# Kernel tuning notes

Measured on AMD Instinct MI355X. Metric: run time of the kernel, lower is better.

Reference implementation:

```python
import jax, jax.numpy as jnp
import numpy as np

N_NODES = 100000
N_EDGES = 1600000
D_IN = 128
D_OUT = 128


def setup_inputs() -> dict:
    key = jax.random.key(0)
    k_x, k_e, k_wl, k_bl, k_wr = jax.random.split(key, 5)
    x = jax.random.normal(k_x, (N_NODES, D_IN), dtype=jnp.float32)
    edge_index = jax.random.randint(k_e, (2, N_EDGES), 0, N_NODES, dtype=jnp.int64)
    s = 1.0 / np.sqrt(D_IN)
    W_l = jax.random.uniform(k_wl, (D_OUT, D_IN), minval=-s, maxval=s, dtype=jnp.float32)
    b_l = jax.random.uniform(k_bl, (D_OUT,), minval=-s, maxval=s, dtype=jnp.float32)
    W_r = jax.random.uniform(k_wr, (D_OUT, D_IN), minval=-s, maxval=s, dtype=jnp.float32)
    return {"x": x, "edge_index": edge_index, "W_l": W_l, "b_l": b_l, "W_r": W_r}


def reference(x, edge_index, W_l, b_l, W_r):
    # PyG SAGEConv with mean aggregation:
    #   out = lin_l(mean_{j in N(i)} x_j) + lin_r(x_i), followed by ReLU.
    src, dst = edge_index[0], edge_index[1]
    # gather source features [E, D_IN] and mean-aggregate at destinations
    msg_sum = jax.ops.segment_sum(x[src], dst, num_segments=N_NODES)  # [N, D_IN]
    deg = jax.ops.segment_sum(jnp.ones((edge_index.shape[1],), dtype=x.dtype), dst,
                              num_segments=N_NODES)  # [N]
    agg = msg_sum / jnp.maximum(deg, 1.0)[:, None]  # isolated nodes -> 0
    out = agg @ W_l.T + b_l + x @ W_r.T
    return jax.nn.relu(out)
```

## Files before the change

### kernel.cpp

```cpp
#include <hip/hip_runtime.h>
#include <hip/hip_bf16.h>
#include <cstddef>
#include <cstdint>

#define D 128
#define BCHUNK 4096
#define SLOTS 64
#define QTILE 64
#define LROW 68
#define GRAN 512
#define SBCAP 9728
#define NGMAX 256

typedef __bf16 bf16x8 __attribute__((ext_vector_type(8)));
typedef float  f32x4  __attribute__((ext_vector_type(4)));
typedef float  f32x2  __attribute__((ext_vector_type(2)));

__device__ __forceinline__ unsigned int f2bf(float f) {
    unsigned int u = __float_as_uint(f);
    return (u + 0x7FFFu + ((u >> 16) & 1u)) >> 16;
}

__global__ __launch_bounds__(256) void bucketx2_kernel(
    const int* __restrict__ ei, int E, int* __restrict__ subCnt,
    unsigned int* __restrict__ sub, int NG, int nbE, int nbX,
    const float4* __restrict__ x4, uint2* __restrict__ xb2,
    unsigned int* __restrict__ xg, int nq,
    const float* __restrict__ Wl, const float* __restrict__ Wr,
    const float* __restrict__ bl, unsigned short* __restrict__ bfrag,
    float* __restrict__ biasbuf)
{
    const int bid = blockIdx.x;
    if (bid >= nbE) {
        const int xi = bid - nbE;
        if (xi < nbX) {
            const int base = xi * 1024 + threadIdx.x;
            #pragma unroll
            for (int k = 0; k < 4; k++) {
                int i = base + k * 256;
                if (i < nq) {
                    float4 v = x4[i];
                    uint2 r;
                    r.x = f2bf(v.x) | (f2bf(v.y) << 16);
                    r.y = f2bf(v.z) | (f2bf(v.w) << 16);
                    xb2[i] = r;
                    int g = 0;
                    g = __builtin_amdgcn_cvt_pk_fp8_f32(v.x, v.y, g, false);
                    g = __builtin_amdgcn_cvt_pk_fp8_f32(v.z, v.w, g, true);
                    xg[(size_t)((i >> 5) + 1) * 32 + (i & 31)] = (unsigned int)g;
                }
            }
        } else {
            int f = (xi - nbX) * 256 + threadIdx.x;
            if (f < 4096) {
                int ct   = f >> 9;
                int q    = (f >> 6) & 7;
                int lane = f & 63;
                int o  = 16 * ct + (lane & 15);
                int kb = 32 * q + (lane >> 4) * 8;
                const float* s = (kb < 128) ? (Wl + (size_t)o * 128 + kb)
                                            : (Wr + (size_t)o * 128 + (kb - 128));
                uint4 u;
                u.x = f2bf(s[0]) | (f2bf(s[1]) << 16);
                u.y = f2bf(s[2]) | (f2bf(s[3]) << 16);
                u.z = f2bf(s[4]) | (f2bf(s[5]) << 16);
                u.w = f2bf(s[6]) | (f2bf(s[7]) << 16);
                reinterpret_cast<uint4*>(bfrag)[f] = u;
                if (f < 128) biasbuf[f] = bl[f];
                if (f < 32)  xg[f] = 0u;
            }
        }
        return;
    }
    __shared__ int cnt[NGMAX];
    __shared__ int basem[NGMAX];
    __shared__ int wsum[4];
    __shared__ unsigned int ebuf[BCHUNK];
    __shared__ unsigned int gpb[BCHUNK];

    for (int i = threadIdx.x; i < NG; i += 256) cnt[i] = 0;
    __syncthreads();
    const int cb = bid * BCHUNK;
    int srcs[16], gs[16], d9s[16];
    #pragma unroll
    for (int k = 0; k < 16; k++) {
        int e = cb + threadIdx.x + k * 256;
        bool v = e < E;
        srcs[k] = v ? ei[e] : 0;
        int dst = v ? ei[E + e] : 0;
        gs[k]  = v ? (dst >> 9) : -1;
        d9s[k] = dst & 511;
        if (v) atomicAdd(&cnt[gs[k]], 1);
    }
    __syncthreads();
    const int tid = threadIdx.x;
    int c = (tid < NG) ? cnt[tid] : 0;
    int gbase = (tid < NG && c > 0) ? atomicAdd(&subCnt[tid], c) : 0;
    int xsc = c;
    #pragma unroll
    for (int dd = 1; dd < 64; dd <<= 1) {
        int y = __shfl_up(xsc, dd);
        if ((tid & 63) >= dd) xsc += y;
    }
    if ((tid & 63) == 63) wsum[tid >> 6] = xsc;
    __syncthreads();
    int woff = 0;
    #pragma unroll
    for (int ww = 0; ww < 4; ww++)
        if (ww < (tid >> 6)) woff += wsum[ww];
    int pref = xsc - c + woff;
    __syncthreads();
    if (tid < NG) { cnt[tid] = pref; basem[tid] = gbase - pref; }
    __syncthreads();
    #pragma unroll
    for (int k = 0; k < 16; k++) {
        if (gs[k] >= 0) {
            int g  = gs[k];
            int lp = atomicAdd(&cnt[g], 1);
            int bp = basem[g] + lp;
            ebuf[lp] = (unsigned int)(srcs[k] + 1) | ((unsigned int)d9s[k] << 20);
            gpb[lp]  = (bp < SBCAP) ? (unsigned int)g * SBCAP + bp : 0xFFFFFFFFu;
        }
    }
    __syncthreads();
    const int nE = min(E - cb, BCHUNK);
    for (int i = tid; i < nE; i += 256) {
        unsigned int p = gpb[i];
        if (p != 0xFFFFFFFFu) sub[p] = ebuf[i];
    }
}

__global__ __launch_bounds__(512) void gathformer_kernel(
    const unsigned int* __restrict__ sub, const int* __restrict__ subCnt,
    const unsigned int* __restrict__ xg, const unsigned int* __restrict__ xb,
    const unsigned short* __restrict__ bfrag, const float* __restrict__ biasbuf,
    float* __restrict__ out, int N)
{
    __shared__ unsigned int lds[QTILE * LROW];
    __shared__ int lcsr[QTILE * SLOTS];
    __shared__ int lcnt[QTILE];

    const int g     = blockIdx.x >> 3;
    const int h     = blockIdx.x & 7;
    const int node0 = g * GRAN + (h << 6);

    const int w    = threadIdx.x >> 6;
    const int lane = threadIdx.x & 63;
    const int sb   = lane & 31;
    const int half = lane >> 5;

    if (threadIdx.x < QTILE) lcnt[threadIdx.x] = 0;
    __syncthreads();
    const int n = min(subCnt[g], SBCAP);
    const unsigned int* S = sub + (size_t)g * SBCAP;
    for (int bi = (int)threadIdx.x * 4; bi < n; bi += 2048) {
        uint4 e4 = *reinterpret_cast<const uint4*>(S + bi);
        #pragma unroll
        for (int j = 0; j < 4; j++) {
            unsigned int en = (&e4.x)[j];
            if (bi + j < n) {
                int d9 = (en >> 20) & 511;
                if ((d9 >> 6) == h) {
                    int ln  = d9 & 63;
                    int pos = atomicAdd(&lcnt[ln], 1);
                    if (pos < SLOTS) lcsr[ln * SLOTS + pos] = (int)(en & 0xFFFFFu);
                }
            }
        }
    }
    __syncthreads();

    const int imax = min(8, N - node0 - w * 8);
    #pragma unroll 2
    for (int i = 0; i < imax; i++) {
        int ln  = w * 8 + i;
        int deg = lcnt[ln];
        int dl  = min(deg, SLOTS);
        int nbatch = (dl + 15) >> 4;
        const int* nb = lcsr + ln * SLOTS;
        f32x2 a01 = {0.f, 0.f};
        f32x2 a23 = {0.f, 0.f};
        for (int b = 0; b < nbatch; b++) {
            const int j = b * 16;
            unsigned int v[8];
            #pragma unroll
            for (int u = 0; u < 8; u++) {
                int slot = j + 2 * u + half;
                int raw  = nb[slot];
                int s    = (slot < dl) ? raw : 0;
                v[u] = xg[(size_t)s * 32 + sb];
            }
            #pragma unroll
            for (int u = 0; u < 8; u++) {
                a01 += __builtin_amdgcn_cvt_pk_f32_fp8(v[u], false);
                a23 += __builtin_amdgcn_cvt_pk_f32_fp8(v[u], true);
            }
        }
        a01.x += __shfl_xor(a01.x, 32);
        a01.y += __shfl_xor(a01.y, 32);
        a23.x += __shfl_xor(a23.x, 32);
        a23.y += __shfl_xor(a23.y, 32);
        if (half == 0) {
            float inv = 1.0f / fmaxf((float)deg, 1.0f);
            int b = ln * LROW + sb * 2;
            lds[b]     = f2bf(a01.x * inv) | (f2bf(a01.y * inv) << 16);
            lds[b + 1] = f2bf(a23.x * inv) | (f2bf(a23.y * inv) << 16);
        }
    }
    __syncthreads();

    const int quad = lane >> 4;
    const int r15  = lane & 15;
    bf16x8 bw[8];
    #pragma unroll
    for (int q = 0; q < 8; q++)
        bw[q] = reinterpret_cast<const bf16x8*>(bfrag)[(w * 8 + q) * 64 + lane];
    const float bias = biasbuf[16 * w + r15];
    const int col = 16 * w + r15;

    #pragma unroll 1
    for (int mt = 0; mt < 4; mt++) {
        int rowbase = node0 + mt * 16;
        if (rowbase >= N) break;
        int rc = min(rowbase + r15, N - 1);
        f32x4 acc = {0.f, 0.f, 0.f, 0.f};
        const int lbase = (mt * 16 + r15) * LROW + quad * 4;
        #pragma unroll
        for (int q = 0; q < 4; q++) {
            bf16x8 a = *reinterpret_cast<const bf16x8*>(&lds[lbase + q * 16]);
            acc = __builtin_amdgcn_mfma_f32_16x16x32_bf16(a, bw[q], acc, 0, 0, 0);
        }
        const unsigned short* xrow =
            (const unsigned short*)xb + (size_t)rc * 128 + quad * 8;
        #pragma unroll
        for (int q = 4; q < 8; q++) {
            bf16x8 a = *reinterpret_cast<const bf16x8*>(xrow + (q - 4) * 32);
            acc = __builtin_amdgcn_mfma_f32_16x16x32_bf16(a, bw[q], acc, 0, 0, 0);
        }
        #pragma unroll
        for (int r = 0; r < 4; r++) {
            int orow = rowbase + quad * 4 + r;
            if (orow < N)
                out[(size_t)orow * D + col] = fmaxf(acc[r] + bias, 0.0f);
        }
    }
}

extern "C" void kernel_launch(void* const* d_in, const int* in_sizes, int n_in,
                              void* d_out, int out_size, void* d_ws, size_t ws_size,
                              hipStream_t stream)
{
    const float* x  = (const float*)d_in[0];
    const int*   ei = (const int*)d_in[1];
    const float* Wl = (const float*)d_in[2];
    const float* bl = (const float*)d_in[3];
    const float* Wr = (const float*)d_in[4];
    float* out = (float*)d_out;

    const int nodes = in_sizes[0] / D;
    const int E     = in_sizes[1] / 2;
    const int NG    = (nodes + GRAN - 1) / GRAN;

    unsigned int* xg = (unsigned int*)d_ws;
    unsigned int* xb = xg + (size_t)(nodes + 1) * 32;
    unsigned short* bfrag = (unsigned short*)(xb + (size_t)nodes * 64);
    float* biasbuf   = (float*)(bfrag + 4096 * 8);
    int* subCnt      = (int*)(biasbuf + 128);
    unsigned int* sub = (unsigned int*)(subCnt + 512);

    hipMemsetAsync(subCnt, 0, (size_t)NG * sizeof(int), stream);

    const int nbE = (E + BCHUNK - 1) / BCHUNK;
    const int nq  = nodes * 32;
    const int nbX = (nq + 1023) / 1024;
    bucketx2_kernel<<<nbE + nbX + 16, 256, 0, stream>>>(
        ei, E, subCnt, sub, NG, nbE, nbX,
        (const float4*)x, (uint2*)xb, xg, nq, Wl, Wr, bl, bfrag, biasbuf);

    gathformer_kernel<<<NG * 8, 512, 0, stream>>>(
        sub, subCnt, xg, xb, bfrag, biasbuf, out, nodes);
}
```

Before: 185.1 us.

## Replace atomic scatter bucketing with chunk-local sort plus deterministic regroup kernel

```diff
diff --git a/kernel.cpp b/kernel.cpp
--- a/kernel.cpp
+++ b/kernel.cpp
@@ -11,6 +11,8 @@
 #define GRAN 512
 #define SBCAP 9728
 #define NGMAX 256
+#define PSTRIDE 200
+#define NBEMAX 416
 
 typedef __bf16 bf16x8 __attribute__((ext_vector_type(8)));
 typedef float  f32x4  __attribute__((ext_vector_type(4)));
@@ -21,9 +23,9 @@
     return (u + 0x7FFFu + ((u >> 16) & 1u)) >> 16;
 }
 
-__global__ __launch_bounds__(256) void bucketx2_kernel(
-    const int* __restrict__ ei, int E, int* __restrict__ subCnt,
-    unsigned int* __restrict__ sub, int NG, int nbE, int nbX,
+__global__ __launch_bounds__(256) void prep_kernel(
+    const int* __restrict__ ei, int E, unsigned int* __restrict__ chunks,
+    unsigned short* __restrict__ pref, int NG, int nbE, int nbX,
     const float4* __restrict__ x4, uint2* __restrict__ xb2,
     unsigned int* __restrict__ xg, int nq,
     const float* __restrict__ Wl, const float* __restrict__ Wr,
@@ -73,14 +75,13 @@
         return;
     }
     __shared__ int cnt[NGMAX];
-    __shared__ int basem[NGMAX];
     __shared__ int wsum[4];
     __shared__ unsigned int ebuf[BCHUNK];
-    __shared__ unsigned int gpb[BCHUNK];
 
     for (int i = threadIdx.x; i < NG; i += 256) cnt[i] = 0;
     __syncthreads();
     const int cb = bid * BCHUNK;
+    const int nE = min(E - cb, BCHUNK);
     int srcs[16], gs[16], d9s[16];
     #pragma unroll
     for (int k = 0; k < 16; k++) {
@@ -95,7 +96,6 @@
     __syncthreads();
     const int tid = threadIdx.x;
     int c = (tid < NG) ? cnt[tid] : 0;
-    int gbase = (tid < NG && c > 0) ? atomicAdd(&subCnt[tid], c) : 0;
     int xsc = c;
     #pragma unroll
     for (int dd = 1; dd < 64; dd <<= 1) {
@@ -108,25 +108,67 @@
     #pragma unroll
     for (int ww = 0; ww < 4; ww++)
         if (ww < (tid >> 6)) woff += wsum[ww];
-    int pref = xsc - c + woff;
-    __syncthreads();
-    if (tid < NG) { cnt[tid] = pref; basem[tid] = gbase - pref; }
+    int pfx = xsc - c + woff;
+    if (tid < NG)  pref[(size_t)bid * PSTRIDE + tid] = (unsigned short)pfx;
+    if (tid == NG) pref[(size_t)bid * PSTRIDE + NG] = (unsigned short)nE;
+    __syncthreads();
+    if (tid < NG) cnt[tid] = pfx;
     __syncthreads();
     #pragma unroll
     for (int k = 0; k < 16; k++) {
         if (gs[k] >= 0) {
-            int g  = gs[k];
-            int lp = atomicAdd(&cnt[g], 1);
-            int bp = basem[g] + lp;
+            int lp = atomicAdd(&cnt[gs[k]], 1);
             ebuf[lp] = (unsigned int)(srcs[k] + 1) | ((unsigned int)d9s[k] << 20);
-            gpb[lp]  = (bp < SBCAP) ? (unsigned int)g * SBCAP + bp : 0xFFFFFFFFu;
-        }
-    }
-    __syncthreads();
-    const int nE = min(E - cb, BCHUNK);
-    for (int i = tid; i < nE; i += 256) {
-        unsigned int p = gpb[i];
-        if (p != 0xFFFFFFFFu) sub[p] = ebuf[i];
+        }
+    }
+    __syncthreads();
+    unsigned int* dst = chunks + (size_t)bid * BCHUNK;
+    #pragma unroll
+    for (int p = 0; p < 4; p++) {
+        int idx = p * 1024 + tid * 4;
+        uint4 v = *reinterpret_cast<const uint4*>(&ebuf[idx]);
+        *reinterpret_cast<uint4*>(&dst[idx]) = v;
+    }
+}
+
+__global__ __launch_bounds__(512) void regroup_kernel(
+    const unsigned int* __restrict__ chunks, const unsigned short* __restrict__ pref,
+    int nbE, unsigned int* __restrict__ sub, int* __restrict__ subCnt, int NG)
+{
+    __shared__ int s_start[NBEMAX], s_off[NBEMAX], s_len[NBEMAX];
+    __shared__ int wsumS[8];
+    const int g    = blockIdx.x;
+    const int tid  = threadIdx.x;
+    const int w    = tid >> 6;
+    const int lane = tid & 63;
+
+    int st = 0, len = 0;
+    if (tid < nbE) {
+        st  = pref[(size_t)tid * PSTRIDE + g];
+        len = pref[(size_t)tid * PSTRIDE + g + 1] - st;
+    }
+    int xsc = len;
+    #pragma unroll
+    for (int dd = 1; dd < 64; dd <<= 1) {
+        int y = __shfl_up(xsc, dd);
+        if (lane >= dd) xsc += y;
+    }
+    if (lane == 63) wsumS[w] = xsc;
+    __syncthreads();
+    int woff = 0;
+    #pragma unroll
+    for (int ww = 0; ww < 8; ww++)
+        if (ww < w) woff += wsumS[ww];
+    int off = xsc - len + woff;
+    if (tid < nbE) { s_start[tid] = st; s_off[tid] = off; s_len[tid] = len; }
+    if (tid == 511) subCnt[g] = off;
+    __syncthreads();
+
+    for (int b = w; b < nbE; b += 8) {
+        int bst = s_start[b], boff = s_off[b], bln = s_len[b];
+        const unsigned int* src = chunks + (size_t)b * BCHUNK + bst;
+        for (int o = lane; o < bln; o += 64)
+            if (boff + o < SBCAP) sub[(size_t)g * SBCAP + boff + o] = src[o];
     }
 }
 
@@ -260,22 +302,24 @@
     const int nodes = in_sizes[0] / D;
     const int E     = in_sizes[1] / 2;
     const int NG    = (nodes + GRAN - 1) / GRAN;
+    const int nbE   = (E + BCHUNK - 1) / BCHUNK;
 
     unsigned int* xg = (unsigned int*)d_ws;
     unsigned int* xb = xg + (size_t)(nodes + 1) * 32;
     unsigned short* bfrag = (unsigned short*)(xb + (size_t)nodes * 64);
     float* biasbuf   = (float*)(bfrag + 4096 * 8);
     int* subCnt      = (int*)(biasbuf + 128);
-    unsigned int* sub = (unsigned int*)(subCnt + 512);
-
-    hipMemsetAsync(subCnt, 0, (size_t)NG * sizeof(int), stream);
-
-    const int nbE = (E + BCHUNK - 1) / BCHUNK;
+    unsigned short* pref = (unsigned short*)(subCnt + 512);
+    unsigned int* chunks = (unsigned int*)(pref + (size_t)nbE * PSTRIDE);
+    unsigned int* sub    = chunks + (size_t)nbE * BCHUNK;
+
     const int nq  = nodes * 32;
     const int nbX = (nq + 1023) / 1024;
-    bucketx2_kernel<<<nbE + nbX + 16, 256, 0, stream>>>(
-        ei, E, subCnt, sub, NG, nbE, nbX,
+    prep_kernel<<<nbE + nbX + 16, 256, 0, stream>>>(
+        ei, E, chunks, pref, NG, nbE, nbX,
         (const float4*)x, (uint2*)xb, xg, nq, Wl, Wr, bl, bfrag, biasbuf);
+
+    regroup_kernel<<<NG, 512, 0, stream>>>(chunks, pref, nbE, sub, subCnt, NG);
 
     gathformer_kernel<<<NG * 8, 512, 0, stream>>>(
         sub, subCnt, xg, xb, bfrag, biasbuf, out, nodes);
```

New measurement: 206.8 us. 1.12x slower.

## Split fused bucket/cast kernel and make gather-transform kernel persistent

Applied to the files above, without the earlier changes.

```diff
diff --git a/kernel.cpp b/kernel.cpp
--- a/kernel.cpp
+++ b/kernel.cpp
@@ -11,6 +11,7 @@
 #define GRAN 512
 #define SBCAP 9728
 #define NGMAX 256
+#define GFGRID 1024
 
 typedef __bf16 bf16x8 __attribute__((ext_vector_type(8)));
 typedef float  f32x4  __attribute__((ext_vector_type(4)));
@@ -21,63 +22,64 @@
     return (u + 0x7FFFu + ((u >> 16) & 1u)) >> 16;
 }
 
-__global__ __launch_bounds__(256) void bucketx2_kernel(
-    const int* __restrict__ ei, int E, int* __restrict__ subCnt,
-    unsigned int* __restrict__ sub, int NG, int nbE, int nbX,
+__global__ __launch_bounds__(256) void xcast_kernel(
     const float4* __restrict__ x4, uint2* __restrict__ xb2,
-    unsigned int* __restrict__ xg, int nq,
+    unsigned int* __restrict__ xg, int nq, int nbX,
     const float* __restrict__ Wl, const float* __restrict__ Wr,
     const float* __restrict__ bl, unsigned short* __restrict__ bfrag,
     float* __restrict__ biasbuf)
 {
-    const int bid = blockIdx.x;
-    if (bid >= nbE) {
-        const int xi = bid - nbE;
-        if (xi < nbX) {
-            const int base = xi * 1024 + threadIdx.x;
-            #pragma unroll
-            for (int k = 0; k < 4; k++) {
-                int i = base + k * 256;
-                if (i < nq) {
-                    float4 v = x4[i];
-                    uint2 r;
-                    r.x = f2bf(v.x) | (f2bf(v.y) << 16);
-                    r.y = f2bf(v.z) | (f2bf(v.w) << 16);
-                    xb2[i] = r;
-                    int g = 0;
-                    g = __builtin_amdgcn_cvt_pk_fp8_f32(v.x, v.y, g, false);
-                    g = __builtin_amdgcn_cvt_pk_fp8_f32(v.z, v.w, g, true);
-                    xg[(size_t)((i >> 5) + 1) * 32 + (i & 31)] = (unsigned int)g;
-                }
-            }
-        } else {
-            int f = (xi - nbX) * 256 + threadIdx.x;
-            if (f < 4096) {
-                int ct   = f >> 9;
-                int q    = (f >> 6) & 7;
-                int lane = f & 63;
-                int o  = 16 * ct + (lane & 15);
-                int kb = 32 * q + (lane >> 4) * 8;
-                const float* s = (kb < 128) ? (Wl + (size_t)o * 128 + kb)
-                                            : (Wr + (size_t)o * 128 + (kb - 128));
-                uint4 u;
-                u.x = f2bf(s[0]) | (f2bf(s[1]) << 16);
-                u.y = f2bf(s[2]) | (f2bf(s[3]) << 16);
-                u.z = f2bf(s[4]) | (f2bf(s[5]) << 16);
-                u.w = f2bf(s[6]) | (f2bf(s[7]) << 16);
-                reinterpret_cast<uint4*>(bfrag)[f] = u;
-                if (f < 128) biasbuf[f] = bl[f];
-                if (f < 32)  xg[f] = 0u;
-            }
-        }
-        return;
-    }
+    const int xi = blockIdx.x;
+    if (xi < nbX) {
+        const int base = xi * 1024 + threadIdx.x;
+        #pragma unroll
+        for (int k = 0; k < 4; k++) {
+            int i = base + k * 256;
+            if (i < nq) {
+                float4 v = x4[i];
+                uint2 r;
+                r.x = f2bf(v.x) | (f2bf(v.y) << 16);
+                r.y = f2bf(v.z) | (f2bf(v.w) << 16);
+                xb2[i] = r;
+                int g = 0;
+                g = __builtin_amdgcn_cvt_pk_fp8_f32(v.x, v.y, g, false);
+                g = __builtin_amdgcn_cvt_pk_fp8_f32(v.z, v.w, g, true);
+                xg[(size_t)((i >> 5) + 1) * 32 + (i & 31)] = (unsigned int)g;
+            }
+        }
+    } else {
+        int f = (xi - nbX) * 256 + threadIdx.x;
+        if (f < 4096) {
+            int ct   = f >> 9;
+            int q    = (f >> 6) & 7;
+            int lane = f & 63;
+            int o  = 16 * ct + (lane & 15);
+            int kb = 32 * q + (lane >> 4) * 8;
+            const float* s = (kb < 128) ? (Wl + (size_t)o * 128 + kb)
+                                        : (Wr + (size_t)o * 128 + (kb - 128));
+            uint4 u;
+            u.x = f2bf(s[0]) | (f2bf(s[1]) << 16);
+            u.y = f2bf(s[2]) | (f2bf(s[3]) << 16);
+            u.z = f2bf(s[4]) | (f2bf(s[5]) << 16);
+            u.w = f2bf(s[6]) | (f2bf(s[7]) << 16);
+            reinterpret_cast<uint4*>(bfrag)[f] = u;
+            if (f < 128) biasbuf[f] = bl[f];
+            if (f < 32)  xg[f] = 0u;
+        }
+    }
+}
+
+__global__ __launch_bounds__(256) void edges_kernel(
+    const int* __restrict__ ei, int E, int* __restrict__ subCnt,
+    unsigned int* __restrict__ sub, int NG)
+{
     __shared__ int cnt[NGMAX];
     __shared__ int basem[NGMAX];
     __shared__ int wsum[4];
     __shared__ unsigned int ebuf[BCHUNK];
     __shared__ unsigned int gpb[BCHUNK];
 
+    const int bid = blockIdx.x;
     for (int i = threadIdx.x; i < NG; i += 256) cnt[i] = 0;
     __syncthreads();
     const int cb = bid * BCHUNK;
@@ -134,115 +136,119 @@
     const unsigned int* __restrict__ sub, const int* __restrict__ subCnt,
     const unsigned int* __restrict__ xg, const unsigned int* __restrict__ xb,
     const unsigned short* __restrict__ bfrag, const float* __restrict__ biasbuf,
-    float* __restrict__ out, int N)
+    float* __restrict__ out, int N, int ntiles)
 {
     __shared__ unsigned int lds[QTILE * LROW];
     __shared__ int lcsr[QTILE * SLOTS];
     __shared__ int lcnt[QTILE];
 
-    const int g     = blockIdx.x >> 3;
-    const int h     = blockIdx.x & 7;
-    const int node0 = g * GRAN + (h << 6);
-
-    const int w    = threadIdx.x >> 6;
-    const int lane = threadIdx.x & 63;
+    const int tid  = threadIdx.x;
+    const int w    = tid >> 6;
+    const int lane = tid & 63;
     const int sb   = lane & 31;
     const int half = lane >> 5;
-
-    if (threadIdx.x < QTILE) lcnt[threadIdx.x] = 0;
-    __syncthreads();
-    const int n = min(subCnt[g], SBCAP);
-    const unsigned int* S = sub + (size_t)g * SBCAP;
-    for (int bi = (int)threadIdx.x * 4; bi < n; bi += 2048) {
-        uint4 e4 = *reinterpret_cast<const uint4*>(S + bi);
-        #pragma unroll
-        for (int j = 0; j < 4; j++) {
-            unsigned int en = (&e4.x)[j];
-            if (bi + j < n) {
-                int d9 = (en >> 20) & 511;
-                if ((d9 >> 6) == h) {
-                    int ln  = d9 & 63;
-                    int pos = atomicAdd(&lcnt[ln], 1);
-                    if (pos < SLOTS) lcsr[ln * SLOTS + pos] = (int)(en & 0xFFFFFu);
-                }
-            }
-        }
-    }
-    __syncthreads();
-
-    const int imax = min(8, N - node0 - w * 8);
-    #pragma unroll 2
-    for (int i = 0; i < imax; i++) {
-        int ln  = w * 8 + i;
-        int deg = lcnt[ln];
-        int dl  = min(deg, SLOTS);
-        int nbatch = (dl + 15) >> 4;
-        const int* nb = lcsr + ln * SLOTS;
-        f32x2 a01 = {0.f, 0.f};
-        f32x2 a23 = {0.f, 0.f};
-        for (int b = 0; b < nbatch; b++) {
-            const int j = b * 16;
-            unsigned int v[8];
-            #pragma unroll
-            for (int u = 0; u < 8; u++) {
-                int slot = j + 2 * u + half;
-                int raw  = nb[slot];
-                int s    = (slot < dl) ? raw : 0;
-                v[u] = xg[(size_t)s * 32 + sb];
-            }
-            #pragma unroll
-            for (int u = 0; u < 8; u++) {
-                a01 += __builtin_amdgcn_cvt_pk_f32_fp8(v[u], false);
-                a23 += __builtin_amdgcn_cvt_pk_f32_fp8(v[u], true);
-            }
-        }
-        a01.x += __shfl_xor(a01.x, 32);
-        a01.y += __shfl_xor(a01.y, 32);
-        a23.x += __shfl_xor(a23.x, 32);
-        a23.y += __shfl_xor(a23.y, 32);
-        if (half == 0) {
-            float inv = 1.0f / fmaxf((float)deg, 1.0f);
-            int b = ln * LROW + sb * 2;
-            lds[b]     = f2bf(a01.x * inv) | (f2bf(a01.y * inv) << 16);
-            lds[b + 1] = f2bf(a23.x * inv) | (f2bf(a23.y * inv) << 16);
-        }
-    }
-    __syncthreads();
-
     const int quad = lane >> 4;
     const int r15  = lane & 15;
-    bf16x8 bw[8];
-    #pragma unroll
-    for (int q = 0; q < 8; q++)
-        bw[q] = reinterpret_cast<const bf16x8*>(bfrag)[(w * 8 + q) * 64 + lane];
-    const float bias = biasbuf[16 * w + r15];
-    const int col = 16 * w + r15;
-
-    #pragma unroll 1
-    for (int mt = 0; mt < 4; mt++) {
-        int rowbase = node0 + mt * 16;
-        if (rowbase >= N) break;
-        int rc = min(rowbase + r15, N - 1);
-        f32x4 acc = {0.f, 0.f, 0.f, 0.f};
-        const int lbase = (mt * 16 + r15) * LROW + quad * 4;
+
+    for (int tile = blockIdx.x; tile < ntiles; tile += gridDim.x) {
+        const int g     = tile >> 3;
+        const int h     = tile & 7;
+        const int node0 = g * GRAN + (h << 6);
+
+        if (tid < QTILE) lcnt[tid] = 0;
+        __syncthreads();
+        const int n = min(subCnt[g], SBCAP);
+        const unsigned int* S = sub + (size_t)g * SBCAP;
+        for (int bi = tid * 4; bi < n; bi += 2048) {
+            uint4 e4 = *reinterpret_cast<const uint4*>(S + bi);
+            #pragma unroll
+            for (int j = 0; j < 4; j++) {
+                unsigned int en = (&e4.x)[j];
+                if (bi + j < n) {
+                    int d9 = (en >> 20) & 511;
+                    if ((d9 >> 6) == h) {
+                        int ln  = d9 & 63;
+                        int pos = atomicAdd(&lcnt[ln], 1);
+                        if (pos < SLOTS) lcsr[ln * SLOTS + pos] = (int)(en & 0xFFFFFu);
+                    }
+                }
+            }
+        }
+        __syncthreads();
+
+        const int imax = min(8, N - node0 - w * 8);
+        #pragma unroll 2
+        for (int i = 0; i < imax; i++) {
+            int ln  = w * 8 + i;
+            int deg = lcnt[ln];
+            int dl  = min(deg, SLOTS);
+            int nbatch = (dl + 15) >> 4;
+            const int* nb = lcsr + ln * SLOTS;
+            f32x2 a01 = {0.f, 0.f};
+            f32x2 a23 = {0.f, 0.f};
+            for (int b = 0; b < nbatch; b++) {
+                const int j = b * 16;
+                unsigned int v[8];
+                #pragma unroll
+                for (int u = 0; u < 8; u++) {
+                    int slot = j + 2 * u + half;
+                    int raw  = nb[slot];
+                    int s    = (slot < dl) ? raw : 0;
+                    v[u] = xg[(size_t)s * 32 + sb];
+                }
+                #pragma unroll
+                for (int u = 0; u < 8; u++) {
+                    a01 += __builtin_amdgcn_cvt_pk_f32_fp8(v[u], false);
+                    a23 += __builtin_amdgcn_cvt_pk_f32_fp8(v[u], true);
+                }
+            }
+            a01.x += __shfl_xor(a01.x, 32);
+            a01.y += __shfl_xor(a01.y, 32);
+            a23.x += __shfl_xor(a23.x, 32);
+            a23.y += __shfl_xor(a23.y, 32);
+            if (half == 0) {
+                float inv = 1.0f / fmaxf((float)deg, 1.0f);
+                int b = ln * LROW + sb * 2;
+                lds[b]     = f2bf(a01.x * inv) | (f2bf(a01.y * inv) << 16);
+                lds[b + 1] = f2bf(a23.x * inv) | (f2bf(a23.y * inv) << 16);
+            }
+        }
+        __syncthreads();
+
+        bf16x8 bw[8];
         #pragma unroll
-        for (int q = 0; q < 4; q++) {
-            bf16x8 a = *reinterpret_cast<const bf16x8*>(&lds[lbase + q * 16]);
-            acc = __builtin_amdgcn_mfma_f32_16x16x32_bf16(a, bw[q], acc, 0, 0, 0);
-        }
-        const unsigned short* xrow =
-            (const unsigned short*)xb + (size_t)rc * 128 + quad * 8;
-        #pragma unroll
-        for (int q = 4; q < 8; q++) {
-            bf16x8 a = *reinterpret_cast<const bf16x8*>(xrow + (q - 4) * 32);
-            acc = __builtin_amdgcn_mfma_f32_16x16x32_bf16(a, bw[q], acc, 0, 0, 0);
-        }
-        #pragma unroll
-        for (int r = 0; r < 4; r++) {
-            int orow = rowbase + quad * 4 + r;
-            if (orow < N)
-                out[(size_t)orow * D + col] = fmaxf(acc[r] + bias, 0.0f);
-        }
+        for (int q = 0; q < 8; q++)
+            bw[q] = reinterpret_cast<const bf16x8*>(bfrag)[(w * 8 + q) * 64 + lane];
+        const float bias = biasbuf[16 * w + r15];
+        const int col = 16 * w + r15;
+
+        #pragma unroll 1
+        for (int mt = 0; mt < 4; mt++) {
+            int rowbase = node0 + mt * 16;
+            if (rowbase >= N) break;
+            int rc = min(rowbase + r15, N - 1);
+            f32x4 acc = {0.f, 0.f, 0.f, 0.f};
+            const int lbase = (mt * 16 + r15) * LROW + quad * 4;
+            #pragma unroll
+            for (int q = 0; q < 4; q++) {
+                bf16x8 a = *reinterpret_cast<const bf16x8*>(&lds[lbase + q * 16]);
+                acc = __builtin_amdgcn_mfma_f32_16x16x32_bf16(a, bw[q], acc, 0, 0, 0);
+            }
+            const unsigned short* xrow =
+                (const unsigned short*)xb + (size_t)rc * 128 + quad * 8;
+            #pragma unroll
+            for (int q = 4; q < 8; q++) {
+                bf16x8 a = *reinterpret_cast<const bf16x8*>(xrow + (q - 4) * 32);
+                acc = __builtin_amdgcn_mfma_f32_16x16x32_bf16(a, bw[q], acc, 0, 0, 0);
+            }
+            #pragma unroll
+            for (int r = 0; r < 4; r++) {
+                int orow = rowbase + quad * 4 + r;
+                if (orow < N)
+                    out[(size_t)orow * D + col] = fmaxf(acc[r] + bias, 0.0f);
+            }
+        }
+        __syncthreads();
     }
 }
 
@@ -260,6 +266,7 @@
     const int nodes = in_sizes[0] / D;
     const int E     = in_sizes[1] / 2;
     const int NG    = (nodes + GRAN - 1) / GRAN;
+    const int nbE   = (E + BCHUNK - 1) / BCHUNK;
 
     unsigned int* xg = (unsigned int*)d_ws;
     unsigned int* xb = xg + (size_t)(nodes + 1) * 32;
@@ -270,13 +277,14 @@
 
     hipMemsetAsync(subCnt, 0, (size_t)NG * sizeof(int), stream);
 
-    const int nbE = (E + BCHUNK - 1) / BCHUNK;
     const int nq  = nodes * 32;
     const int nbX = (nq + 1023) / 1024;
-    bucketx2_kernel<<<nbE + nbX + 16, 256, 0, stream>>>(
-        ei, E, subCnt, sub, NG, nbE, nbX,
-        (const float4*)x, (uint2*)xb, xg, nq, Wl, Wr, bl, bfrag, biasbuf);
-
-    gathformer_kernel<<<NG * 8, 512, 0, stream>>>(
-        sub, subCnt, xg, xb, bfrag, biasbuf, out, nodes);
-}
+    xcast_kernel<<<nbX + 16, 256, 0, stream>>>(
+        (const float4*)x, (uint2*)xb, xg, nq, nbX, Wl, Wr, bl, bfrag, biasbuf);
+
+    edges_kernel<<<nbE, 256, 0, stream>>>(ei, E, subCnt, sub, NG);
+
+    const int ntiles = NG * 8;
+    gathformer_kernel<<<min(ntiles, GFGRID), 512, 0, stream>>>(
+        sub, subCnt, xg, xb, bfrag, biasbuf, out, nodes, ntiles);
+}
```

New measurement: 210.3 us. 1.14x slower.
